# Performance work log

Hardware: AMD Instinct MI355X
Metric: run time of the kernel (lower is better)

Reference implementation:

```python
import jax, jax.numpy as jnp
import numpy as np

N_EMBD = 64
N_HEAD = 4
HEAD_DIM = N_EMBD // N_HEAD  # 16


def setup_inputs() -> dict:
    key = jax.random.key(0)
    ks = jax.random.split(key, 4)
    B, T = 1024, 128
    x = jax.random.normal(ks[0], (B, T, N_EMBD), dtype=jnp.float32)
    W_attn = jax.random.normal(ks[1], (N_EMBD, 3 * N_EMBD), dtype=jnp.float32) * (1.0 / np.sqrt(N_EMBD))
    b_attn = jnp.zeros((3 * N_EMBD,), dtype=jnp.float32)
    W_proj = jax.random.normal(ks[2], (N_EMBD, N_EMBD), dtype=jnp.float32) * (1.0 / np.sqrt(N_EMBD))
    b_proj = jnp.zeros((N_EMBD,), dtype=jnp.float32)
    return {"x": x, "W_attn": W_attn, "b_attn": b_attn, "W_proj": W_proj, "b_proj": b_proj}


def reference(x, W_attn, b_attn, W_proj, b_proj):
    B, T, C = x.shape
    qkv = x @ W_attn + b_attn                      # [B,T,3C]
    q, k, v = jnp.split(qkv, 3, axis=-1)
    # [B,T,C] -> [B,H,T,D]
    q = q.reshape(B, T, N_HEAD, HEAD_DIM).transpose(0, 2, 1, 3)
    k = k.reshape(B, T, N_HEAD, HEAD_DIM).transpose(0, 2, 1, 3)
    v = v.reshape(B, T, N_HEAD, HEAD_DIM).transpose(0, 2, 1, 3)
    att = jnp.einsum('bhtd,bhsd->bhts', q, k) * (HEAD_DIM ** -0.5)  # [B,H,T,T]
    causal = jnp.tril(jnp.ones((T, T), dtype=bool))
    att = jnp.where(causal[None, None], att, -jnp.inf)
    att = jax.nn.softmax(att, axis=-1)
    # dropout is identity in eval mode (reference uses eval semantics)
    y = jnp.einsum('bhts,bhsd->bhtd', att, v)       # [B,H,T,D]
    y = y.transpose(0, 2, 1, 3).reshape(B, T, C)
    return y @ W_proj + b_proj
```

## Files before the change

### kernel.cpp

```cpp
#include <hip/hip_runtime.h>
#include <hip/hip_fp16.h>

#define NTH 256

typedef __attribute__((ext_vector_type(4))) _Float16 f16x4;
typedef __attribute__((ext_vector_type(8))) _Float16 f16x8;
typedef __attribute__((ext_vector_type(4))) float f32x4;

union U16x8 { uint4 u; f16x8 h; };
union U16x4 { uint2 u; f16x4 h; };

static __device__ __forceinline__ unsigned pk2(float a, float b) {
    union { __half2 h; unsigned u; } v;
    v.h = __floats2half2_rn(a, b);
    return v.u;
}
static __device__ __forceinline__ f16x4 pk4(f32x4 v) {
    U16x4 r; r.u = make_uint2(pk2(v[0], v[1]), pk2(v[2], v[3]));
    return r.h;
}
static __device__ __forceinline__ f16x8 ld2b64(const _Float16* p) {
    uint2 lo = *reinterpret_cast<const uint2*>(p);
    uint2 hi = *reinterpret_cast<const uint2*>(p + 4);
    U16x8 r; r.u = make_uint4(lo.x, lo.y, hi.x, hi.y);
    return r.h;
}
static __device__ __forceinline__ f16x8 w_frag(const float* __restrict__ p, int stride, float scale) {
    f16x8 f;
    #pragma unroll
    for (int j = 0; j < 8; ++j) f[j] = (_Float16)(p[j * stride] * scale);
    return f;
}

template<int N0, int N1, int N2, int N3, int NKV>
static __device__ __forceinline__ void attn_quad(
    const f16x4* __restrict__ Kf, const f16x4* __restrict__ Vf,
    const f16x4* __restrict__ Qf, _Float16* __restrict__ sO,
    int lc, int lg, int h)
{
    constexpr int Ns[4] = {N0, N1, N2, N3};

    f32x4 Of[4];
    float l[4];
    #pragma unroll
    for (int u = 0; u < 4; ++u) { Of[u] = (f32x4){0.f, 0.f, 0.f, 0.f}; l[u] = 0.f; }

    #pragma unroll
    for (int st = 0; st < NKV; ++st) {
        #pragma unroll
        for (int u = 0; u < 4; ++u) {
            if (st > Ns[u]) continue;
            f32x4 z = (f32x4){0.f, 0.f, 0.f, 0.f};
            f32x4 sf = __builtin_amdgcn_mfma_f32_16x16x16f16(Kf[st], Qf[Ns[u]], z, 0, 0, 0);
            float e[4];
            #pragma unroll
            for (int j = 0; j < 4; ++j) {
                float sv = sf[j];
                if (st == Ns[u]) sv = (4 * lg + j <= lc) ? sv : -1e30f;
                e[j] = __builtin_amdgcn_exp2f(sv);
            }
            l[u] += (e[0] + e[1]) + (e[2] + e[3]);
            f32x4 ef = (f32x4){e[0], e[1], e[2], e[3]};
            Of[u] = __builtin_amdgcn_mfma_f32_16x16x16f16(Vf[st], pk4(ef), Of[u], 0, 0, 0);
        }
    }

    #pragma unroll
    for (int u = 0; u < 4; ++u) {
        float lu = l[u];
        lu += __shfl_xor(lu, 16);
        lu += __shfl_xor(lu, 32);
        float inv = __fdividef(1.0f, lu);
        uint2 ou = make_uint2(pk2(Of[u][0] * inv, Of[u][1] * inv),
                              pk2(Of[u][2] * inv, Of[u][3] * inv));
        *reinterpret_cast<uint2*>(sO + (16 * Ns[u] + lc) * 76 + 16 * h + 4 * lg) = ou;
    }
}

__global__ __launch_bounds__(NTH, 4)
void csa_fused(const float* __restrict__ x, const float* __restrict__ Wa,
               const float* __restrict__ ba, const float* __restrict__ Wp,
               const float* __restrict__ bp, float* __restrict__ out)
{
    __shared__ _Float16 sx[128 * 72];
    __shared__ _Float16 sO[128 * 76];

    const int b    = blockIdx.x;
    const int tid  = threadIdx.x;
    const int lane = tid & 63;
    const int w    = tid >> 6;
    const int lc   = lane & 15;
    const int lg   = lane >> 4;
    const int h    = w;

    const float* __restrict__ xb = x + (size_t)b * 8192;

    #pragma unroll
    for (int e = 0; e < 8; ++e) {
        int f = tid + NTH * e;
        int r = f >> 4, c = (f & 15) << 2;
        float4 v4 = *reinterpret_cast<const float4*>(xb + r * 64 + c);
        U16x4 u; u.u = make_uint2(pk2(v4.x, v4.y), pk2(v4.z, v4.w));
        *reinterpret_cast<f16x4*>(sx + r * 72 + c) = u.h;
    }

    const float QSC = 0.25f * 1.44269504088896f;
    f16x8 wq[2], wk[2], wv[2];
    #pragma unroll
    for (int kk = 0; kk < 2; ++kk) {
        const float* wa_k = Wa + (size_t)(32 * kk + 8 * lg) * 192;
        wq[kk] = w_frag(wa_k + 16 * h + lc,       192, QSC);
        wk[kk] = w_frag(wa_k + 64 + 16 * h + lc,  192, 1.0f);
        wv[kk] = w_frag(wa_k + 128 + 16 * h + lc, 192, 1.0f);
    }
    float4 bq = *reinterpret_cast<const float4*>(ba + 16 * h + 4 * lg);
    bq.x *= QSC; bq.y *= QSC; bq.z *= QSC; bq.w *= QSC;
    const float4 bk = *reinterpret_cast<const float4*>(ba + 64 + 16 * h + 4 * lg);
    const float  bv = ba[128 + 16 * h + lc];

    __syncthreads();

    f16x4 Kf[8], Vf[8], Qf[8];
    #pragma unroll
    for (int M = 0; M < 8; ++M) {
        f16x8 xf0 = *reinterpret_cast<const f16x8*>(sx + (16 * M + lc) * 72 + 8 * lg);
        f16x8 xf1 = *reinterpret_cast<const f16x8*>(sx + (16 * M + lc) * 72 + 32 + 8 * lg);

        f32x4 ka = (f32x4){bk.x, bk.y, bk.z, bk.w};
        ka = __builtin_amdgcn_mfma_f32_16x16x32_f16(wk[0], xf0, ka, 0, 0, 0);
        ka = __builtin_amdgcn_mfma_f32_16x16x32_f16(wk[1], xf1, ka, 0, 0, 0);
        Kf[M] = pk4(ka);

        f32x4 va = (f32x4){bv, bv, bv, bv};
        va = __builtin_amdgcn_mfma_f32_16x16x32_f16(xf0, wv[0], va, 0, 0, 0);
        va = __builtin_amdgcn_mfma_f32_16x16x32_f16(xf1, wv[1], va, 0, 0, 0);
        Vf[M] = pk4(va);

        f32x4 qa = (f32x4){bq.x, bq.y, bq.z, bq.w};
        qa = __builtin_amdgcn_mfma_f32_16x16x32_f16(wq[0], xf0, qa, 0, 0, 0);
        qa = __builtin_amdgcn_mfma_f32_16x16x32_f16(wq[1], xf1, qa, 0, 0, 0);
        Qf[M] = pk4(qa);
    }

    attn_quad<0, 3, 4, 7, 8>(Kf, Vf, Qf, sO, lc, lg, h);
    attn_quad<1, 2, 5, 6, 7>(Kf, Vf, Qf, sO, lc, lg, h);

    const int m = w;
    f16x8 af[2];
    #pragma unroll
    for (int kk = 0; kk < 2; ++kk)
        af[kk] = w_frag(Wp + (size_t)(32 * kk + 8 * lg) * 64 + 16 * m + lc, 64, 1.0f);
    const float4 bia = *reinterpret_cast<const float4*>(bp + 16 * m + 4 * lg);

    __syncthreads();

    {
        f32x4 dacc[8];
        #pragma unroll
        for (int t = 0; t < 8; ++t) dacc[t] = (f32x4){bia.x, bia.y, bia.z, bia.w};

        #pragma unroll
        for (int kk = 0; kk < 2; ++kk) {
            #pragma unroll
            for (int t = 0; t < 8; ++t) {
                f16x8 bf = ld2b64(sO + (16 * t + lc) * 76 + 32 * kk + 8 * lg);
                dacc[t] = __builtin_amdgcn_mfma_f32_16x16x32_f16(af[kk], bf, dacc[t], 0, 0, 0);
            }
        }
        #pragma unroll
        for (int t = 0; t < 8; ++t) {
            int tt = 16 * t + lc;
            *reinterpret_cast<float4*>(out + (size_t)b * 8192 + tt * 64 + 16 * m + 4 * lg) =
                make_float4(dacc[t][0], dacc[t][1], dacc[t][2], dacc[t][3]);
        }
    }
}

extern "C" void kernel_launch(void* const* d_in, const int* in_sizes, int n_in,
                              void* d_out, int out_size, void* d_ws, size_t ws_size,
                              hipStream_t stream) {
    const float* x  = (const float*)d_in[0];
    const float* Wa = (const float*)d_in[1];
    const float* ba = (const float*)d_in[2];
    const float* Wp = (const float*)d_in[3];
    const float* bp = (const float*)d_in[4];
    float* out = (float*)d_out;

    const int B = in_sizes[0] / 8192;

    csa_fused<<<B, NTH, 0, stream>>>(x, Wa, ba, Wp, bp, out);
}
```

Measured before the change: 23.25 us.

## Split each batch into two query-half blocks to double grid parallelism

Launches 2*B blocks, each covering one half of the query rows of a batch element. The first-half block loads and projects only the first 64 tokens, while the second-half block loads all 128 tokens for K/V and computes Q only for its own rows. A single shared buffer is reused for both x staging and the attention output to cut LDS use. The goal is better occupancy and load balance across CUs. The cost is recomputing the first-half K/V projection in the second block and extra reads of x.

New measurement: 42.98 us. +84.9%, slower.

```diff
diff --git a/kernel.cpp b/kernel.cpp
--- a/kernel.cpp
+++ b/kernel.cpp
@@ -32,13 +32,48 @@
     return f;
 }
 
-template<int N0, int N1, int N2, int N3, int NKV>
-static __device__ __forceinline__ void attn_quad(
-    const f16x4* __restrict__ Kf, const f16x4* __restrict__ Vf,
-    const f16x4* __restrict__ Qf, _Float16* __restrict__ sO,
-    int lc, int lg, int h)
+template<int P>
+static __device__ __forceinline__ void half_attn(
+    const float* __restrict__ xb, _Float16* __restrict__ sx, _Float16* __restrict__ sO,
+    const f16x8* wq, const f16x8* wk, const f16x8* wv,
+    float4 bq, float4 bk, float bv, int tid, int lc, int lg, int h)
 {
-    constexpr int Ns[4] = {N0, N1, N2, N3};
+    constexpr int NKV = 4 * (P + 1);
+
+    #pragma unroll
+    for (int e = 0; e < NKV; ++e) {
+        int f = tid + NTH * e;
+        int r = f >> 4, c = (f & 15) << 2;
+        float4 v4 = *reinterpret_cast<const float4*>(xb + r * 64 + c);
+        U16x4 u; u.u = make_uint2(pk2(v4.x, v4.y), pk2(v4.z, v4.w));
+        *reinterpret_cast<f16x4*>(sx + r * 72 + c) = u.h;
+    }
+    __syncthreads();
+
+    f16x4 Kf[NKV], Vf[NKV], Qf[4];
+    #pragma unroll
+    for (int M = 0; M < NKV; ++M) {
+        f16x8 xf0 = *reinterpret_cast<const f16x8*>(sx + (16 * M + lc) * 72 + 8 * lg);
+        f16x8 xf1 = *reinterpret_cast<const f16x8*>(sx + (16 * M + lc) * 72 + 32 + 8 * lg);
+
+        f32x4 ka = (f32x4){bk.x, bk.y, bk.z, bk.w};
+        ka = __builtin_amdgcn_mfma_f32_16x16x32_f16(wk[0], xf0, ka, 0, 0, 0);
+        ka = __builtin_amdgcn_mfma_f32_16x16x32_f16(wk[1], xf1, ka, 0, 0, 0);
+        Kf[M] = pk4(ka);
+
+        f32x4 va = (f32x4){bv, bv, bv, bv};
+        va = __builtin_amdgcn_mfma_f32_16x16x32_f16(xf0, wv[0], va, 0, 0, 0);
+        va = __builtin_amdgcn_mfma_f32_16x16x32_f16(xf1, wv[1], va, 0, 0, 0);
+        Vf[M] = pk4(va);
+
+        if (M >= NKV - 4) {
+            f32x4 qa = (f32x4){bq.x, bq.y, bq.z, bq.w};
+            qa = __builtin_amdgcn_mfma_f32_16x16x32_f16(wq[0], xf0, qa, 0, 0, 0);
+            qa = __builtin_amdgcn_mfma_f32_16x16x32_f16(wq[1], xf1, qa, 0, 0, 0);
+            Qf[M - (NKV - 4)] = pk4(qa);
+        }
+    }
+    __syncthreads();
 
     f32x4 Of[4];
     float l[4];
@@ -49,14 +84,14 @@
     for (int st = 0; st < NKV; ++st) {
         #pragma unroll
         for (int u = 0; u < 4; ++u) {
-            if (st > Ns[u]) continue;
+            if (st > 4 * P + u) continue;
             f32x4 z = (f32x4){0.f, 0.f, 0.f, 0.f};
-            f32x4 sf = __builtin_amdgcn_mfma_f32_16x16x16f16(Kf[st], Qf[Ns[u]], z, 0, 0, 0);
+            f32x4 sf = __builtin_amdgcn_mfma_f32_16x16x16f16(Kf[st], Qf[u], z, 0, 0, 0);
             float e[4];
             #pragma unroll
             for (int j = 0; j < 4; ++j) {
                 float sv = sf[j];
-                if (st == Ns[u]) sv = (4 * lg + j <= lc) ? sv : -1e30f;
+                if (st == 4 * P + u) sv = (4 * lg + j <= lc) ? sv : -1e30f;
                 e[j] = __builtin_amdgcn_exp2f(sv);
             }
             l[u] += (e[0] + e[1]) + (e[2] + e[3]);
@@ -73,19 +108,20 @@
         float inv = __fdividef(1.0f, lu);
         uint2 ou = make_uint2(pk2(Of[u][0] * inv, Of[u][1] * inv),
                               pk2(Of[u][2] * inv, Of[u][3] * inv));
-        *reinterpret_cast<uint2*>(sO + (16 * Ns[u] + lc) * 76 + 16 * h + 4 * lg) = ou;
+        *reinterpret_cast<uint2*>(sO + (16 * u + lc) * 76 + 16 * h + 4 * lg) = ou;
     }
 }
 
 __global__ __launch_bounds__(NTH, 4)
 void csa_fused(const float* __restrict__ x, const float* __restrict__ Wa,
                const float* __restrict__ ba, const float* __restrict__ Wp,
-               const float* __restrict__ bp, float* __restrict__ out)
+               const float* __restrict__ bp, float* __restrict__ out, int B)
 {
-    __shared__ _Float16 sx[128 * 72];
-    __shared__ _Float16 sO[128 * 76];
+    __shared__ _Float16 sbuf[128 * 72];
 
-    const int b    = blockIdx.x;
+    const int idx  = blockIdx.x;
+    const int p    = (idx >= B) ? 1 : 0;
+    const int b    = idx - p * B;
     const int tid  = threadIdx.x;
     const int lane = tid & 63;
     const int w    = tid >> 6;
@@ -94,15 +130,6 @@
     const int h    = w;
 
     const float* __restrict__ xb = x + (size_t)b * 8192;
-
-    #pragma unroll
-    for (int e = 0; e < 8; ++e) {
-        int f = tid + NTH * e;
-        int r = f >> 4, c = (f & 15) << 2;
-        float4 v4 = *reinterpret_cast<const float4*>(xb + r * 64 + c);
-        U16x4 u; u.u = make_uint2(pk2(v4.x, v4.y), pk2(v4.z, v4.w));
-        *reinterpret_cast<f16x4*>(sx + r * 72 + c) = u.h;
-    }
 
     const float QSC = 0.25f * 1.44269504088896f;
     f16x8 wq[2], wk[2], wv[2];
@@ -118,32 +145,10 @@
     const float4 bk = *reinterpret_cast<const float4*>(ba + 64 + 16 * h + 4 * lg);
     const float  bv = ba[128 + 16 * h + lc];
 
-    __syncthreads();
-
-    f16x4 Kf[8], Vf[8], Qf[8];
-    #pragma unroll
-    for (int M = 0; M < 8; ++M) {
-        f16x8 xf0 = *reinterpret_cast<const f16x8*>(sx + (16 * M + lc) * 72 + 8 * lg);
-        f16x8 xf1 = *reinterpret_cast<const f16x8*>(sx + (16 * M + lc) * 72 + 32 + 8 * lg);
-
-        f32x4 ka = (f32x4){bk.x, bk.y, bk.z, bk.w};
-        ka = __builtin_amdgcn_mfma_f32_16x16x32_f16(wk[0], xf0, ka, 0, 0, 0);
-        ka = __builtin_amdgcn_mfma_f32_16x16x32_f16(wk[1], xf1, ka, 0, 0, 0);
-        Kf[M] = pk4(ka);
-
-        f32x4 va = (f32x4){bv, bv, bv, bv};
-        va = __builtin_amdgcn_mfma_f32_16x16x32_f16(xf0, wv[0], va, 0, 0, 0);
-        va = __builtin_amdgcn_mfma_f32_16x16x32_f16(xf1, wv[1], va, 0, 0, 0);
-        Vf[M] = pk4(va);
-
-        f32x4 qa = (f32x4){bq.x, bq.y, bq.z, bq.w};
-        qa = __builtin_amdgcn_mfma_f32_16x16x32_f16(wq[0], xf0, qa, 0, 0, 0);
-        qa = __builtin_amdgcn_mfma_f32_16x16x32_f16(wq[1], xf1, qa, 0, 0, 0);
-        Qf[M] = pk4(qa);
-    }
-
-    attn_quad<0, 3, 4, 7, 8>(Kf, Vf, Qf, sO, lc, lg, h);
-    attn_quad<1, 2, 5, 6, 7>(Kf, Vf, Qf, sO, lc, lg, h);
+    if (p == 0)
+        half_attn<0>(xb, sbuf, sbuf, wq, wk, wv, bq, bk, bv, tid, lc, lg, h);
+    else
+        half_attn<1>(xb, sbuf, sbuf, wq, wk, wv, bq, bk, bv, tid, lc, lg, h);
 
     const int m = w;
     f16x8 af[2];
@@ -155,22 +160,23 @@
     __syncthreads();
 
     {
-        f32x4 dacc[8];
+        f32x4 dacc[4];
         #pragma unroll
-        for (int t = 0; t < 8; ++t) dacc[t] = (f32x4){bia.x, bia.y, bia.z, bia.w};
+        for (int t = 0; t < 4; ++t) dacc[t] = (f32x4){bia.x, bia.y, bia.z, bia.w};
 
         #pragma unroll
         for (int kk = 0; kk < 2; ++kk) {
             #pragma unroll
-            for (int t = 0; t < 8; ++t) {
-                f16x8 bf = ld2b64(sO + (16 * t + lc) * 76 + 32 * kk + 8 * lg);
+            for (int t = 0; t < 4; ++t) {
+                f16x8 bf = ld2b64(sbuf + (16 * t + lc) * 76 + 32 * kk + 8 * lg);
                 dacc[t] = __builtin_amdgcn_mfma_f32_16x16x32_f16(af[kk], bf, dacc[t], 0, 0, 0);
             }
         }
+        float* ob = out + (size_t)b * 8192 + (size_t)(64 * p) * 64;
         #pragma unroll
-        for (int t = 0; t < 8; ++t) {
+        for (int t = 0; t < 4; ++t) {
             int tt = 16 * t + lc;
-            *reinterpret_cast<float4*>(out + (size_t)b * 8192 + tt * 64 + 16 * m + 4 * lg) =
+            *reinterpret_cast<float4*>(ob + tt * 64 + 16 * m + 4 * lg) =
                 make_float4(dacc[t][0], dacc[t][1], dacc[t][2], dacc[t][3]);
         }
     }
@@ -188,5 +194,5 @@
 
     const int B = in_sizes[0] / 8192;
 
-    csa_fused<<<B, NTH, 0, stream>>>(x, Wa, ba, Wp, bp, out);
+    csa_fused<<<2 * B, NTH, 0, stream>>>(x, Wa, ba, Wp, bp, out, B);
 }
```
